# Kernel tuning notes

Hardware: AMD Instinct MI355X
Metric: run time of the kernel (lower is better)

## Reference

```python
import jax, jax.numpy as jnp
from jax import lax
import numpy as np


def _pool_matrix(L, S):
    # AdaptiveAvgPool1d(L -> S): output i averages input [floor(i*L/S), ceil((i+1)*L/S))
    P = np.zeros((S, L), dtype=np.float32)
    for i in range(S):
        s = (i * L) // S
        e = -(-((i + 1) * L) // S)
        P[i, s:e] = 1.0 / (e - s)
    return jnp.asarray(P)


def _gmask_index(Lc, kind):
    idx = jnp.arange(Lc, dtype=jnp.float32)
    ref = float((Lc + 1) // 2 if kind == 'center' else Lc - 1)
    sigma = jnp.mean(jnp.abs(idx - ref))
    w = jnp.exp(-0.5 * (idx - ref) ** 2 / sigma ** 2)
    return w / w.sum()  # (Lc,)


def _gmask_vector(seq, kind):
    Lc = seq.shape[1]
    ref_i = (Lc + 1) // 2 if kind == 'center' else Lc - 1
    diff = seq - seq[:, ref_i, :][:, None, :]
    d = jnp.sqrt(jnp.maximum(jnp.sum(diff * diff, axis=2), 1e-12))  # safe ||.||2
    sigma = jnp.mean(d, axis=1, keepdims=True)
    w = jnp.exp(-0.5 * (d / sigma) ** 2)
    return w / jnp.sum(w, axis=1, keepdims=True)  # (B, Lc)


def _l2norm(w):  # F.normalize(p=2, dim=1)
    return w / jnp.maximum(jnp.linalg.norm(w, axis=1, keepdims=True), 1e-12)


def _dwconv(u, w, b, L):
    # u: (B, len, C); depthwise Conv1d, padding=d_conv-1 both sides, slice [:, :, :L]
    C = u.shape[-1]
    pad = w.shape[-1] - 1
    v = lax.conv_general_dilated(u.transpose(0, 2, 1), w, (1,), [(pad, pad)],
                                 dimension_numbers=('NCH', 'OIH', 'NCH'),
                                 feature_group_count=C)
    v = v + b[None, :, None]
    return v[:, :, :L].transpose(0, 2, 1)


def _ssm(u, W_xp, b_xp, W_dt, b_dt, A_log, D):
    d_state = A_log.shape[1]
    dt_rank = W_dt.shape[1]
    A = -jnp.exp(A_log)                                       # (d_inner, d_state)
    dbc = u @ W_xp.T + b_xp
    dr = dbc[..., :dt_rank]
    Bm = dbc[..., dt_rank:dt_rank + d_state]
    Cm = dbc[..., dt_rank + d_state:]
    delta = jax.nn.softplus(dr @ W_dt.T + b_dt)               # (B, L, d_inner)
    deltaA = jnp.exp(delta[..., None] * A)                    # (B, L, d_inner, d_state)
    BX = (delta * u)[..., None] * Bm[:, :, None, :]           # (B, L, d_inner, d_state)

    def comb(e1, e2):  # h_t = a_t * h_{t-1} + b_t (parallel scan)
        a1, b1 = e1
        a2, b2 = e2
        return a1 * a2, a2 * b1 + b2

    hs = lax.associative_scan(comb, (deltaA, BX), axis=1)[1]
    return jnp.einsum('blds,bls->bld', hs, Cm) + D * u


def _forward(x, W_in_x, W_in_z, conv_w_f, conv_b_f, conv_w_b, conv_b_b,
             W_xp_f, b_xp_f, W_dt_f, b_dt_f, A_log_f, D_f,
             W_xp_b, b_xp_b, W_dt_b, b_dt_b, A_log_b, D_b,
             W_pro_to, b_pro_to, token_wA, token_wV, W_out):
    B, L, Dm = x.shape
    S = token_wA.shape[1]
    xi = x @ W_in_x.T
    z = x @ W_in_z.T
    mid = L // 2 + 1
    x_f = xi[:, :mid]
    x_b = xi[:, mid - 1:][:, ::-1]
    x_f = jax.nn.silu(_dwconv(x_f, conv_w_f, conv_b_f, L))
    x_b = jax.nn.silu(_dwconv(x_b, conv_w_b, conv_b_b, L))
    y_f = _ssm(x_f, W_xp_f, b_xp_f, W_dt_f, b_dt_f, A_log_f, D_f)
    y_b = _ssm(x_b, W_xp_b, b_xp_b, W_dt_b, b_dt_b, A_log_b, D_b)
    Lc = y_f.shape[1]
    m_f = _l2norm(_gmask_index(Lc, 'last')[None, :] * _gmask_vector(y_f, 'last'))
    m_b = _l2norm(_gmask_index(Lc, 'last')[None, :] * _gmask_vector(y_b, 'last'))
    y_cat = jnp.concatenate([y_f * m_f[..., None], y_b * m_b[:, ::-1, None]], axis=-1)
    y = y_cat @ W_pro_to.T + b_pro_to
    m = _l2norm(_gmask_index(Lc, 'center')[None, :] * _gmask_vector(y, 'center'))
    y = y * m[..., None]
    # tokenizer (direction 'f'), dropout is identity at eval
    Atok = jax.nn.softmax(jnp.einsum('bld,td->btl', y, token_wA[0]), axis=-1)
    VV = jnp.einsum('bld,de->ble', y, token_wV[0])
    T = jnp.einsum('btl,ble->bte', Atok, VV)
    # z branch: adaptive avg pool L -> S then silu
    P = _pool_matrix(L, S)
    zp = jax.nn.silu(jnp.einsum('bld,sl->bsd', z, P))
    return (T * zp) @ W_out.T


def setup_inputs() -> dict:
    key = jax.random.key(0)
    B, L, D = 8, 2049, 256
    d_inner, d_state, dt_rank, d_conv, S = 512, 16, 16, 4, 64
    ks = jax.random.split(key, 20)
    rn = lambda k, sh, sc: jax.random.normal(k, sh, jnp.float32) * sc
    A_log = jnp.tile(jnp.log(jnp.arange(1.0, d_state + 1.0, dtype=jnp.float32))[None, :], (d_inner, 1))
    return {
        'x': rn(ks[0], (B, L, D), 1.0),
        'W_in_x': rn(ks[1], (d_inner, D), D ** -0.5),
        'W_in_z': rn(ks[2], (d_inner, D), D ** -0.5),
        'conv_w_f': rn(ks[3], (d_inner, 1, d_conv), 0.5),
        'conv_b_f': rn(ks[4], (d_inner,), 0.1),
        'conv_w_b': rn(ks[5], (d_inner, 1, d_conv), 0.5),
        'conv_b_b': rn(ks[6], (d_inner,), 0.1),
        'W_xp_f': rn(ks[7], (dt_rank + 2 * d_state, d_inner), d_inner ** -0.5),
        'b_xp_f': rn(ks[8], (dt_rank + 2 * d_state,), 0.02),
        'W_dt_f': rn(ks[9], (d_inner, dt_rank), dt_rank ** -0.5),
        'b_dt_f': jax.random.uniform(ks[10], (d_inner,), jnp.float32, -4.0, -2.0),
        'A_log_f': A_log,
        'D_f': jnp.ones((d_inner,), jnp.float32),
        'W_xp_b': rn(ks[11], (dt_rank + 2 * d_state, d_inner), d_inner ** -0.5),
        'b_xp_b': rn(ks[12], (dt_rank + 2 * d_state,), 0.02),
        'W_dt_b': rn(ks[13], (d_inner, dt_rank), dt_rank ** -0.5),
        'b_dt_b': jax.random.uniform(ks[14], (d_inner,), jnp.float32, -4.0, -2.0),
        'A_log_b': A_log,
        'D_b': jnp.ones((d_inner,), jnp.float32),
        'W_pro_to': rn(ks[15], (d_inner, 2 * d_inner), (2 * d_inner) ** -0.5),
        'b_pro_to': jnp.zeros((d_inner,), jnp.float32),
        'token_wA': rn(ks[16], (1, S, d_inner), (2.0 / d_inner) ** 0.5),
        'token_wV': rn(ks[17], (1, d_inner, d_inner), (2.0 / d_inner) ** 0.5),
        'W_out': rn(ks[18], (D, d_inner), d_inner ** -0.5),
    }


def reference(x, W_in_x, W_in_z, conv_w_f, conv_b_f, conv_w_b, conv_b_b,
              W_xp_f, b_xp_f, W_dt_f, b_dt_f, A_log_f, D_f,
              W_xp_b, b_xp_b, W_dt_b, b_dt_b, A_log_b, D_b,
              W_pro_to, b_pro_to, token_wA, token_wV, W_out):
    return _forward(x, W_in_x, W_in_z, conv_w_f, conv_b_f, conv_w_b, conv_b_b,
                    W_xp_f, b_xp_f, W_dt_f, b_dt_f, A_log_f, D_f,
                    W_xp_b, b_xp_b, W_dt_b, b_dt_b, A_log_b, D_b,
                    W_pro_to, b_pro_to, token_wA, token_wV, W_out)
```

## Files before the change

kernel.cpp:

```cpp
#include <hip/hip_runtime.h>
#include <math.h>

#define BB 8
#define LL 2049
#define DD 256
#define EE 512
#define NS 16
#define LC 1028
#define SS 64
#define SC 40
#define CH 26
#define LN2F 0.6931471805599453f

typedef __attribute__((ext_vector_type(8))) short short8x;
typedef __attribute__((ext_vector_type(4))) float f32x4;

__device__ __forceinline__ float4 ld4g(const float* p) { return *(const float4*)p; }

__device__ __forceinline__ unsigned short bfrne(float f)
{
    unsigned int u = __float_as_uint(f);
    unsigned int r = (u + 0x7FFFu + ((u >> 16) & 1u)) >> 16;
    return (unsigned short)r;
}

__device__ __forceinline__ float fast_softplus(float x)
{
    float sp = __log2f(1.f + __expf(x)) * LN2F;
    return x > 8.f ? x + __expf(-x) : sp;
}

__device__ __forceinline__ float fast_silu(float x)
{
    return __fdividef(x, 1.f + __expf(-x));
}

__device__ __forceinline__ void gl_lds16(const unsigned short* g, unsigned short* l)
{
    __builtin_amdgcn_global_load_lds(
        (const __attribute__((address_space(1))) unsigned int*)g,
        (__attribute__((address_space(3))) unsigned int*)l, 16, 0, 0);
}

__device__ __forceinline__ void gemm_bf16_core(
    unsigned short* As, unsigned short* Bs,
    const unsigned short* __restrict__ A, const unsigned short* __restrict__ Bw,
    const float* __restrict__ bias, float* __restrict__ C,
    int M, int N, int K, int ldc)
{
    const int tid = threadIdx.x;
    const int wave = tid >> 6, lane = tid & 63;
    const int quad = lane >> 4, l16 = lane & 15;
    const int m0 = blockIdx.y * 128, n0 = blockIdx.x * 128;
    const int wm = (wave >> 1) * 64, wn = (wave & 1) * 64;
    const int srow = lane >> 2;
    const int skoff = (lane & 3) * 8;

    f32x4 acc[4][4];
#pragma unroll
    for (int i = 0; i < 4; i++)
#pragma unroll
        for (int j = 0; j < 4; j++) { f32x4 z = {0.f, 0.f, 0.f, 0.f}; acc[i][j] = z; }

    for (int k0 = 0; k0 < K; k0 += 32) {
#pragma unroll
        for (int half = 0; half < 2; half++) {
            int r = wave * 32 + half * 16 + srow;
            int ga = m0 + r; if (ga > M - 1) ga = M - 1;
            int gb = n0 + r; if (gb > N - 1) gb = N - 1;
            gl_lds16(A + (size_t)ga * K + k0 + skoff, &As[(wave * 32 + half * 16) * 32]);
            gl_lds16(Bw + (size_t)gb * K + k0 + skoff, &Bs[(wave * 32 + half * 16) * 32]);
        }
        __syncthreads();
        short8x af[4], bf[4];
#pragma unroll
        for (int t = 0; t < 4; t++) {
            af[t] = *(const short8x*)&As[(wm + t * 16 + l16) * 32 + quad * 8];
            bf[t] = *(const short8x*)&Bs[(wn + t * 16 + l16) * 32 + quad * 8];
        }
#pragma unroll
        for (int mt = 0; mt < 4; mt++)
#pragma unroll
            for (int nt = 0; nt < 4; nt++)
                acc[mt][nt] = __builtin_amdgcn_mfma_f32_16x16x32_bf16(
                    af[mt], bf[nt], acc[mt][nt], 0, 0, 0);
        __syncthreads();
    }

#pragma unroll
    for (int mt = 0; mt < 4; mt++) {
#pragma unroll
        for (int r = 0; r < 4; r++) {
            int m = m0 + wm + mt * 16 + quad * 4 + r;
            if (m >= M) continue;
#pragma unroll
            for (int nt = 0; nt < 4; nt++) {
                int n = n0 + wn + nt * 16 + l16;
                if (n >= N) continue;
                float v = acc[mt][nt][r];
                if (bias) v += bias[n];
                C[(size_t)m * ldc + n] = v;
            }
        }
    }
}

__global__ __launch_bounds__(256) void gemm_bf16_bt(
    const unsigned short* __restrict__ A, const unsigned short* __restrict__ Bw,
    const float* __restrict__ bias, float* __restrict__ C,
    int M, int N, int K, int ldc)
{
    __shared__ unsigned short As[128 * 32];
    __shared__ unsigned short Bs[128 * 32];
    gemm_bf16_core(As, Bs, A, Bw, bias, C, M, N, K, ldc);
}

__global__ __launch_bounds__(256) void gemm_bf16_pair(
    const unsigned short* __restrict__ A0, const unsigned short* __restrict__ A1,
    const unsigned short* __restrict__ B0, const unsigned short* __restrict__ B1,
    const float* __restrict__ bias0, const float* __restrict__ bias1,
    float* __restrict__ C0, float* __restrict__ C1,
    int M, int N, int K, int ldc)
{
    __shared__ unsigned short As[128 * 32];
    __shared__ unsigned short Bs[128 * 32];
    int z = blockIdx.z;
    gemm_bf16_core(As, Bs, z ? A1 : A0, z ? B1 : B0, z ? bias1 : bias0,
                   z ? C1 : C0, M, N, K, ldc);
}

__global__ __launch_bounds__(256) void cvt_all(
    const float* __restrict__ s0, unsigned short* __restrict__ d0,
    const float* __restrict__ s1, unsigned short* __restrict__ d1,
    const float* __restrict__ s2, unsigned short* __restrict__ d2,
    const float* __restrict__ s3, unsigned short* __restrict__ d3,
    const float* __restrict__ s4, unsigned short* __restrict__ d4,
    const float* __restrict__ s5, unsigned short* __restrict__ d5,
    const float* __restrict__ s6, unsigned short* __restrict__ d6,
    const float* __restrict__ sV, unsigned short* __restrict__ dV)
{
    __shared__ float tile[32][33];
    if (blockIdx.x < 1024) {
        const size_t c0 = 1049088, c1 = c0 + 32768, c2 = c1 + 32768, c3 = c2 + 6144,
                     c4 = c3 + 6144, c5 = c4 + 131072, c6 = c5 + 8192;
        size_t stride = (size_t)1024 * 256;
        for (size_t i = (size_t)blockIdx.x * 256 + threadIdx.x; i < c6; i += stride) {
            const float* s; unsigned short* d; size_t j;
            if (i < c0)      { s = s0; d = d0; j = i; }
            else if (i < c1) { s = s1; d = d1; j = i - c0; }
            else if (i < c2) { s = s2; d = d2; j = i - c1; }
            else if (i < c3) { s = s3; d = d3; j = i - c2; }
            else if (i < c4) { s = s4; d = d4; j = i - c3; }
            else if (i < c5) { s = s5; d = d5; j = i - c4; }
            else             { s = s6; d = d6; j = i - c5; }
            float4 v = ((const float4*)s)[j];
            ushort4 o;
            o.x = bfrne(v.x); o.y = bfrne(v.y); o.z = bfrne(v.z); o.w = bfrne(v.w);
            ((ushort4*)d)[j] = o;
        }
    } else {
        int t = blockIdx.x - 1024;
        int bx = t & 15, by = t >> 4;
        int tx = threadIdx.x & 31, ty = threadIdx.x >> 5;
        for (int i = 0; i < 32; i += 8)
            tile[ty + i][tx] = sV[(size_t)(by * 32 + ty + i) * 512 + bx * 32 + tx];
        __syncthreads();
        for (int i = 0; i < 32; i += 8)
            dV[(size_t)(bx * 32 + ty + i) * 512 + by * 32 + tx] = bfrne(tile[tx][ty + i]);
    }
}

__global__ __launch_bounds__(256) void gemm_abt(
    const float* __restrict__ A, const float* __restrict__ Bw,
    const float* __restrict__ bias, float* __restrict__ C,
    float* __restrict__ Cpart, int M, int N, int K)
{
    __shared__ float As[16][132];
    __shared__ float Bs[16][132];
    const int tid = threadIdx.x;
    const int tx = tid & 15, ty = tid >> 4;
    const int m0 = blockIdx.y * 128, n0 = blockIdx.x * 128;
    const int Ks = K / gridDim.z;
    const int kbeg = blockIdx.z * Ks, kend = kbeg + Ks;
    const int r0 = tid >> 2, r1 = r0 + 64;
    const int kc = (tid & 3) * 4;

    float acc[8][8];
#pragma unroll
    for (int i = 0; i < 8; i++)
#pragma unroll
        for (int j = 0; j < 8; j++) acc[i][j] = 0.f;

    const float4 z4 = make_float4(0.f, 0.f, 0.f, 0.f);
    float4 a0, a1, b0, b1;
    a0 = (m0 + r0 < M) ? ld4g(A + (size_t)(m0 + r0) * K + kbeg + kc) : z4;
    a1 = (m0 + r1 < M) ? ld4g(A + (size_t)(m0 + r1) * K + kbeg + kc) : z4;
    b0 = (n0 + r0 < N) ? ld4g(Bw + (size_t)(n0 + r0) * K + kbeg + kc) : z4;
    b1 = (n0 + r1 < N) ? ld4g(Bw + (size_t)(n0 + r1) * K + kbeg + kc) : z4;

    for (int k0 = kbeg; k0 < kend; k0 += 16) {
        As[kc + 0][r0] = a0.x; As[kc + 1][r0] = a0.y; As[kc + 2][r0] = a0.z; As[kc + 3][r0] = a0.w;
        As[kc + 0][r1] = a1.x; As[kc + 1][r1] = a1.y; As[kc + 2][r1] = a1.z; As[kc + 3][r1] = a1.w;
        Bs[kc + 0][r0] = b0.x; Bs[kc + 1][r0] = b0.y; Bs[kc + 2][r0] = b0.z; Bs[kc + 3][r0] = b0.w;
        Bs[kc + 0][r1] = b1.x; Bs[kc + 1][r1] = b1.y; Bs[kc + 2][r1] = b1.z; Bs[kc + 3][r1] = b1.w;
        __syncthreads();
        if ((k0 + 16) < kend) {
            int kn = k0 + 16 + kc;
            a0 = (m0 + r0 < M) ? ld4g(A + (size_t)(m0 + r0) * K + kn) : z4;
            a1 = (m0 + r1 < M) ? ld4g(A + (size_t)(m0 + r1) * K + kn) : z4;
            b0 = (n0 + r0 < N) ? ld4g(Bw + (size_t)(n0 + r0) * K + kn) : z4;
            b1 = (n0 + r1 < N) ? ld4g(Bw + (size_t)(n0 + r1) * K + kn) : z4;
        }
#pragma unroll
        for (int kk = 0; kk < 16; kk++) {
            float4 alo = *(const float4*)&As[kk][ty * 4];
            float4 ahi = *(const float4*)&As[kk][64 + ty * 4];
            float4 blo = *(const float4*)&Bs[kk][tx * 4];
            float4 bhi = *(const float4*)&Bs[kk][64 + tx * 4];
            float a[8] = {alo.x, alo.y, alo.z, alo.w, ahi.x, ahi.y, ahi.z, ahi.w};
            float b[8] = {blo.x, blo.y, blo.z, blo.w, bhi.x, bhi.y, bhi.z, bhi.w};
#pragma unroll
            for (int i = 0; i < 8; i++)
#pragma unroll
                for (int j = 0; j < 8; j++) acc[i][j] += a[i] * b[j];
        }
        __syncthreads();
    }

    float* Co = (blockIdx.z == 0) ? C : Cpart + (size_t)(blockIdx.z - 1) * M * N;
    const bool addb = (bias != nullptr) && (blockIdx.z == 0);
#pragma unroll
    for (int i = 0; i < 8; i++) {
        int m = m0 + (i < 4 ? ty * 4 + i : 64 + ty * 4 + i - 4);
        if (m >= M) continue;
#pragma unroll
        for (int jh = 0; jh < 2; jh++) {
            int n = n0 + jh * 64 + tx * 4;
            if (n >= N) continue;
            float4 o;
            o.x = acc[i][jh * 4 + 0]; o.y = acc[i][jh * 4 + 1];
            o.z = acc[i][jh * 4 + 2]; o.w = acc[i][jh * 4 + 3];
            if (addb) {
                o.x += bias[n]; o.y += bias[n + 1];
                o.z += bias[n + 2]; o.w += bias[n + 3];
            }
            *(float4*)(Co + (size_t)m * N + n) = o;
        }
    }
}

__global__ __launch_bounds__(256) void reduce_add(
    float* __restrict__ C, const float* __restrict__ P, int parts, size_t total)
{
    size_t stride = (size_t)gridDim.x * 256 * 4;
    for (size_t i = ((size_t)blockIdx.x * 256 + threadIdx.x) * 4; i < total; i += stride) {
        float4 c = *(float4*)(C + i);
        for (int p = 0; p < parts; p++) {
            float4 v = *(const float4*)(P + (size_t)p * total + i);
            c.x += v.x; c.y += v.y; c.z += v.z; c.w += v.w;
        }
        *(float4*)(C + i) = c;
    }
}

__global__ __launch_bounds__(256) void conv_silu_kernel(
    const float* __restrict__ xi,
    const float* __restrict__ wf, const float* __restrict__ bf,
    const float* __restrict__ wb, const float* __restrict__ bbk,
    float* __restrict__ xfc, float* __restrict__ xbc,
    unsigned short* __restrict__ xfcbf, unsigned short* __restrict__ xbcbf)
{
    int idx = blockIdx.x * 256 + threadIdx.x;
    if (idx >= LC * EE) return;
    int b = blockIdx.y;
    int dir = blockIdx.z;
    int t = idx >> 9;
    int e = idx & 511;
    const float* w = dir ? wb : wf;
    float s = dir ? bbk[e] : bf[e];
#pragma unroll
    for (int k = 0; k < 4; k++) {
        int j = t + k - 3;
        if (j >= 0 && j <= 1024) {
            int src_l = dir ? (2048 - j) : j;
            s += w[e * 4 + k] * xi[((size_t)b * LL + src_l) * EE + e];
        }
    }
    float v = fast_silu(s);
    size_t o = ((size_t)b * LC + t) * EE + e;
    (dir ? xbc : xfc)[o] = v;
    (dir ? xbcbf : xfcbf)[o] = bfrne(v);
}

__device__ __forceinline__ void pow_tree(float r, float* pw)
{
    float r2 = r * r;
    float r4 = r2 * r2;
    float r8 = r4 * r4;
    pw[0] = r;        pw[1] = r2;       pw[2] = r2 * r;   pw[3] = r4;
    pw[4] = r4 * r;   pw[5] = r4 * r2;  pw[6] = r4 * pw[2]; pw[7] = r8;
    pw[8] = r8 * r;   pw[9] = r8 * r2;  pw[10] = r8 * pw[2]; pw[11] = r8 * r4;
    pw[12] = r8 * pw[4]; pw[13] = r8 * pw[5]; pw[14] = r8 * pw[6]; pw[15] = r8 * r8;
}

__global__ __launch_bounds__(256) void scan_phase1(
    const float* __restrict__ xfc, const float* __restrict__ xbc,
    const float* __restrict__ dbcf, const float* __restrict__ dbcb,
    const float* __restrict__ Wdt_f, const float* __restrict__ bdt_f,
    const float* __restrict__ Alog_f,
    const float* __restrict__ Wdt_b, const float* __restrict__ bdt_b,
    const float* __restrict__ Alog_b,
    float* __restrict__ Hloc, float* __restrict__ Dsum)
{
    const int bid = blockIdx.x;
    const int half = bid & 1;
    const int c = (bid >> 1) % SC;
    const int rest = (bid >> 1) / SC;
    const int b = rest & 7;
    const int dir = rest >> 3;
    const int e = half * 256 + threadIdx.x;

    const float* u    = dir ? xbc : xfc;
    const float* dbc  = dir ? dbcb : dbcf;
    const float* Wdt  = dir ? Wdt_b : Wdt_f;
    const float* bdt  = dir ? bdt_b : bdt_f;
    const float* Alog = dir ? Alog_b : Alog_f;

    float W[16], h[16];
#pragma unroll
    for (int i = 0; i < 16; i += 4) {
        float4 w4 = *(const float4*)(Wdt + e * 16 + i);
        W[i] = w4.x; W[i + 1] = w4.y; W[i + 2] = w4.z; W[i + 3] = w4.w;
    }
#pragma unroll
    for (int i = 0; i < 16; i++) h[i] = 0.f;
    float A0 = -__expf(Alog[e * 16]);
    float bd = bdt[e];
    float dsum = 0.f;

    const int l0 = c * CH;
    int l1 = l0 + CH; if (l1 > LC) l1 = LC;
    const float* urow = u + ((size_t)b * LC + l0) * EE + e;
    const float* row  = dbc + ((size_t)b * LC + l0) * 48;

    for (int l = l0; l < l1; ++l, row += 48, urow += EE) {
        float p = bd;
#pragma unroll
        for (int k = 0; k < 16; k++) p += row[k] * W[k];
        float delta = fast_softplus(p);
        dsum += delta;
        float du = delta * (*urow);
        float r = __expf(delta * A0);
        float pw[16];
        pow_tree(r, pw);
#pragma unroll
        for (int n = 0; n < 16; n++) h[n] = pw[n] * h[n] + du * row[16 + n];
    }
    size_t base = ((((size_t)dir * 8 + b) * SC + c) * 16) * 512 + e;
#pragma unroll
    for (int n = 0; n < 16; n++) Hloc[base + (size_t)n * 512] = h[n];
    Dsum[(((size_t)dir * 8 + b) * SC + c) * 512 + e] = dsum;
}

__global__ __launch_bounds__(256) void scan_phase2(
    float* __restrict__ Hloc, const float* __restrict__ Dsum,
    const float* __restrict__ Alog_f, const float* __restrict__ Alog_b)
{
    int gid = blockIdx.x * 256 + threadIdx.x;
    int e = gid & 511;
    int n = (gid >> 9) & 15;
    int b = (gid >> 13) & 7;
    int dir = gid >> 16;
    const float* Alog = dir ? Alog_b : Alog_f;
    float An = -__expf(Alog[e * 16 + n]);
    size_t base = (((size_t)dir * 8 + b) * SC * 16 + n) * 512 + e;
    size_t dbase = ((size_t)dir * 8 + b) * SC * 512 + e;
    float h = 0.f;
#pragma unroll
    for (int c = 0; c < SC; c++) {
        size_t off = base + (size_t)c * 16 * 512;
        float tmp = Hloc[off];
        float P = __expf(Dsum[dbase + (size_t)c * 512] * An);
        Hloc[off] = h;
        h = P * h + tmp;
    }
}

__global__ __launch_bounds__(256) void scan_phase3(
    const float* __restrict__ xfc, const float* __restrict__ xbc,
    const float* __restrict__ dbcf, const float* __restrict__ dbcb,
    const float* __restrict__ Wdt_f, const float* __restrict__ bdt_f,
    const float* __restrict__ Alog_f, const float* __restrict__ Df,
    const float* __restrict__ Wdt_b, const float* __restrict__ bdt_b,
    const float* __restrict__ Alog_b, const float* __restrict__ Db,
    const float* __restrict__ Hin,
    float* __restrict__ yf, float* __restrict__ yb)
{
    const int bid = blockIdx.x;
    const int half = bid & 1;
    const int c = (bid >> 1) % SC;
    const int rest = (bid >> 1) / SC;
    const int b = rest & 7;
    const int dir = rest >> 3;
    const int e = half * 256 + threadIdx.x;

    const float* u    = dir ? xbc : xfc;
    const float* dbc  = dir ? dbcb : dbcf;
    const float* Wdt  = dir ? Wdt_b : Wdt_f;
    const float* bdt  = dir ? bdt_b : bdt_f;
    const float* Alog = dir ? Alog_b : Alog_f;
    const float* Dp   = dir ? Db : Df;
    float* y          = dir ? yb : yf;

    float W[16], h[16];
#pragma unroll
    for (int i = 0; i < 16; i += 4) {
        float4 w4 = *(const float4*)(Wdt + e * 16 + i);
        W[i] = w4.x; W[i + 1] = w4.y; W[i + 2] = w4.z; W[i + 3] = w4.w;
    }
    float A0 = -__expf(Alog[e * 16]);
    float bd = bdt[e];
    float Dv = Dp[e];
    size_t hbase = ((((size_t)dir * 8 + b) * SC + c) * 16) * 512 + e;
#pragma unroll
    for (int n = 0; n < 16; n++) h[n] = Hin[hbase + (size_t)n * 512];

    const int l0 = c * CH;
    int l1 = l0 + CH; if (l1 > LC) l1 = LC;
    const float* urow = u + ((size_t)b * LC + l0) * EE + e;
    float* yrow       = y + ((size_t)b * LC + l0) * EE + e;
    const float* row  = dbc + ((size_t)b * LC + l0) * 48;

    for (int l = l0; l < l1; ++l, row += 48, urow += EE, yrow += EE) {
        float p = bd;
#pragma unroll
        for (int k = 0; k < 16; k++) p += row[k] * W[k];
        float delta = fast_softplus(p);
        float uv = *urow;
        float du = delta * uv;
        float r = __expf(delta * A0);
        float pw[16];
        pow_tree(r, pw);
        float q0 = 0.f, q1 = 0.f, q2 = 0.f, q3 = 0.f;
#pragma unroll
        for (int i = 0; i < 4; i++) {
#pragma unroll
            for (int j = 0; j < 4; j++) {
                int n = i * 4 + j;
                h[n] = pw[n] * h[n] + du * row[16 + n];
            }
            q0 += h[i * 4 + 0] * row[32 + i * 4 + 0];
            q1 += h[i * 4 + 1] * row[32 + i * 4 + 1];
            q2 += h[i * 4 + 2] * row[32 + i * 4 + 2];
            q3 += h[i * 4 + 3] * row[32 + i * 4 + 3];
        }
        *yrow = ((q0 + q1) + (q2 + q3)) + Dv * uv;
    }
}

__global__ __launch_bounds__(256) void dist2_kernel(
    const float* __restrict__ Y0, const float* __restrict__ Y1,
    float* __restrict__ D0, float* __restrict__ D1, int ref_l)
{
    const float* Y = blockIdx.z ? Y1 : Y0;
    float* dbuf = blockIdx.z ? D1 : D0;
    int wave = threadIdx.x >> 6;
    int lane = threadIdx.x & 63;
    int l = blockIdx.x * 4 + wave;
    int b = blockIdx.y;
    if (l >= LC) return;
    const float* row = Y + ((size_t)b * LC + l) * EE;
    const float* ref = Y + ((size_t)b * LC + ref_l) * EE;
    float s = 0.f;
#pragma unroll
    for (int i = 0; i < 8; i += 4) {
        float4 a = *(const float4*)(row + lane * 8 + i);
        float4 r = *(const float4*)(ref + lane * 8 + i);
        float dx = a.x - r.x, dy = a.y - r.y, dz = a.z - r.z, dw = a.w - r.w;
        s += dx * dx + dy * dy + dz * dz + dw * dw;
    }
    for (int m = 1; m < 64; m <<= 1) s += __shfl_xor(s, m, 64);
    if (lane == 0) dbuf[(size_t)b * LC + l] = sqrtf(fmaxf(s, 1e-12f));
}

__device__ __forceinline__ float block_reduce_sum256(float v, float* red)
{
    int tid = threadIdx.x;
    red[tid] = v; __syncthreads();
    for (int s = 128; s > 0; s >>= 1) {
        if (tid < s) red[tid] += red[tid + s];
        __syncthreads();
    }
    float r = red[0]; __syncthreads();
    return r;
}

__global__ __launch_bounds__(256) void mask_finalize2(
    const float* __restrict__ db0, const float* __restrict__ db1,
    float* __restrict__ mb0, float* __restrict__ mb1, float ref)
{
    __shared__ float red[256];
    int b = blockIdx.x, tid = threadIdx.x;
    const float* d = (blockIdx.y ? db1 : db0) + (size_t)b * LC;
    float* m = (blockIdx.y ? mb1 : mb0) + (size_t)b * LC;
    float s1 = 0.f, s2 = 0.f;
    for (int l = tid; l < LC; l += 256) {
        s1 += d[l];
        s2 += fabsf((float)l - ref);
    }
    float sigma = block_reduce_sum256(s1, red) / (float)LC;
    float si    = block_reduce_sum256(s2, red) / (float)LC;
    float invsg = 1.f / sigma, invsi = 1.f / si;
    float s3 = 0.f, s4 = 0.f;
    for (int l = tid; l < LC; l += 256) {
        float t1 = d[l] * invsg;             s3 += __expf(-0.5f * t1 * t1);
        float t2 = ((float)l - ref) * invsi; s4 += __expf(-0.5f * t2 * t2);
    }
    float invwv = 1.f / block_reduce_sum256(s3, red);
    float invwi = 1.f / block_reduce_sum256(s4, red);
    float s5 = 0.f;
    for (int l = tid; l < LC; l += 256) {
        float t1 = d[l] * invsg;             float gv = __expf(-0.5f * t1 * t1) * invwv;
        float t2 = ((float)l - ref) * invsi; float gi = __expf(-0.5f * t2 * t2) * invwi;
        float v = gi * gv; s5 += v * v;
    }
    float invn = 1.f / fmaxf(sqrtf(block_reduce_sum256(s5, red)), 1e-12f);
    for (int l = tid; l < LC; l += 256) {
        float t1 = d[l] * invsg;             float gv = __expf(-0.5f * t1 * t1) * invwv;
        float t2 = ((float)l - ref) * invsi; float gi = __expf(-0.5f * t2 * t2) * invwi;
        m[l] = (gi * gv) * invn;
    }
}

__global__ __launch_bounds__(256) void build_ycat_bf16(
    const float* __restrict__ yf, const float* __restrict__ yb,
    const float* __restrict__ mf, const float* __restrict__ mb,
    unsigned short* __restrict__ ycat)
{
    size_t idx = (size_t)blockIdx.x * 256 + threadIdx.x;
    if (idx >= (size_t)BB * LC * EE) return;
    int e = (int)(idx & 511);
    size_t bl = idx >> 9;
    int l = (int)(bl % LC);
    int b = (int)(bl / LC);
    size_t rl = (size_t)b * LC + (LC - 1 - l);
    ycat[bl * 1024 + e] = bfrne(yf[idx] * mf[bl]);
    ycat[bl * 1024 + 512 + e] = bfrne(yb[idx] * mb[rl]);
}

__global__ __launch_bounds__(256) void apply_mask_bf16(
    const float* __restrict__ y, const float* __restrict__ mc,
    unsigned short* __restrict__ ybf)
{
    size_t idx = (size_t)blockIdx.x * 256 + threadIdx.x;
    if (idx >= (size_t)BB * LC * EE) return;
    ybf[idx] = bfrne(y[idx] * mc[idx >> 9]);
}

__global__ __launch_bounds__(256) void softmax_l(float* __restrict__ logits)
{
    __shared__ float red[256];
    int b = blockIdx.x >> 6, t = blockIdx.x & 63;
    int tid = threadIdx.x;
    float* base = logits + (size_t)b * LC * 576 + t;
    float mx = -1e30f;
    for (int l = tid; l < LC; l += 256) mx = fmaxf(mx, base[(size_t)l * 576]);
    red[tid] = mx; __syncthreads();
    for (int s = 128; s > 0; s >>= 1) {
        if (tid < s) red[tid] = fmaxf(red[tid], red[tid + s]);
        __syncthreads();
    }
    mx = red[0]; __syncthreads();
    float sum = 0.f;
    for (int l = tid; l < LC; l += 256) sum += __expf(base[(size_t)l * 576] - mx);
    red[tid] = sum; __syncthreads();
    for (int s = 128; s > 0; s >>= 1) {
        if (tid < s) red[tid] += red[tid + s];
        __syncthreads();
    }
    float inv = 1.f / red[0];
    for (int l = tid; l < LC; l += 256)
        base[(size_t)l * 576] = __expf(base[(size_t)l * 576] - mx) * inv;
}

__global__ __launch_bounds__(256) void t_kernel(
    const float* __restrict__ cc, const float* __restrict__ zp,
    float* __restrict__ T)
{
    __shared__ float As[16][64];
    int b = blockIdx.y;
    int e0 = blockIdx.x * 64;
    int lbeg = blockIdx.z * 129;
    int lend = lbeg + 129; if (lend > LC) lend = LC;
    int tid = threadIdx.x;
    int el = tid & 63;
    int tq = tid >> 6;
    float acc[16];
#pragma unroll
    for (int j = 0; j < 16; j++) acc[j] = 0.f;
    for (int l0 = lbeg; l0 < lend; l0 += 16) {
        int lld = tid >> 4;
        int tld = (tid & 15) * 4;
        int l = l0 + lld;
        float4 v = make_float4(0.f, 0.f, 0.f, 0.f);
        if (l < lend) v = *(const float4*)(cc + ((size_t)b * LC + l) * 576 + tld);
        *(float4*)&As[lld][tld] = v;
        __syncthreads();
        int lmax = lend - l0 < 16 ? lend - l0 : 16;
        for (int i = 0; i < lmax; i++) {
            float vvv = cc[((size_t)b * LC + l0 + i) * 576 + 64 + e0 + el];
#pragma unroll
            for (int j = 0; j < 16; j++) acc[j] += As[i][tq * 16 + j] * vvv;
        }
        __syncthreads();
    }
#pragma unroll
    for (int j = 0; j < 16; j++) {
        size_t o = ((size_t)b * 64 + tq * 16 + j) * EE + e0 + el;
        atomicAdd(&T[o], acc[j] * zp[o]);
    }
}

__global__ __launch_bounds__(256) void zp_kernel(
    const float* __restrict__ z, float* __restrict__ zp, float* __restrict__ T)
{
    int s = blockIdx.x, b = blockIdx.y;
    int tid = threadIdx.x;
    {
        size_t base = ((size_t)b * SS + s) * 512;
        *(float4*)(T + base + tid * 2) = make_float4(0.f, 0.f, 0.f, 0.f);
    }
    int si = (s * LL) / SS;
    int ei = ((s + 1) * LL + SS - 1) / SS;
    float inv = 1.f / (float)(ei - si);
    for (int d = tid; d < EE; d += 256) {
        float acc = 0.f;
        for (int l = si; l < ei; l++) acc += z[((size_t)b * LL + l) * EE + d];
        zp[((size_t)b * SS + s) * EE + d] = fast_silu(acc * inv);
    }
}

extern "C" void kernel_launch(void* const* d_in, const int* in_sizes, int n_in,
                              void* d_out, int out_size, void* d_ws, size_t ws_size,
                              hipStream_t stream)
{
    const float* x        = (const float*)d_in[0];
    const float* W_in_x   = (const float*)d_in[1];
    const float* W_in_z   = (const float*)d_in[2];
    const float* conv_w_f = (const float*)d_in[3];
    const float* conv_b_f = (const float*)d_in[4];
    const float* conv_w_b = (const float*)d_in[5];
    const float* conv_b_b = (const float*)d_in[6];
    const float* W_xp_f   = (const float*)d_in[7];
    const float* b_xp_f   = (const float*)d_in[8];
    const float* W_dt_f   = (const float*)d_in[9];
    const float* b_dt_f   = (const float*)d_in[10];
    const float* A_log_f  = (const float*)d_in[11];
    const float* D_f      = (const float*)d_in[12];
    const float* W_xp_b   = (const float*)d_in[13];
    const float* b_xp_b   = (const float*)d_in[14];
    const float* W_dt_b   = (const float*)d_in[15];
    const float* b_dt_b   = (const float*)d_in[16];
    const float* A_log_b  = (const float*)d_in[17];
    const float* D_b      = (const float*)d_in[18];
    const float* W_pro    = (const float*)d_in[19];
    const float* b_pro    = (const float*)d_in[20];
    const float* token_wA = (const float*)d_in[21];
    const float* token_wV = (const float*)d_in[22];
    const float* W_out    = (const float*)d_in[23];
    float* out = (float*)d_out;
    float* ws  = (float*)d_ws;

    const size_t n1 = (size_t)BB * LL * EE;
    const size_t n2 = (size_t)BB * LC * EE;
    const size_t n3 = (size_t)BB * LC * 48;
    const size_t n4 = (size_t)BB * LC;
    const size_t n6 = (size_t)BB * SS * EE;
    const size_t nHl = (size_t)2 * BB * SC * 16 * 512;

    float* z_buf  = ws;
    float* xi     = z_buf + n1;
    float* xfc    = xi + n1;
    float* xbc    = xfc + n2;
    float* dbcf   = xbc + n2;
    float* dbcb   = dbcf + n3;
    float* yb_buf = dbcb + n3;
    float* y_buf  = yb_buf + n2;
    float* mf     = y_buf + n2;
    float* mb     = mf + n4;
    float* mc     = mb + n4;
    float* d1     = mc + n4;
    float* d2     = d1 + n4;
    float* T_buf  = d2 + n4;
    float* zp_buf = T_buf + n6;
    float* wA_reg = zp_buf + n6;
    float* wvt_reg = wA_reg + 16384;
    size_t need = (size_t)(wvt_reg + 131072 - ws) * sizeof(float);
    if (ws_size < need) return;

    float* Hloc   = xi;
    float* Dsum   = xi + nHl;
    float* Cc     = xi;
    float* yf_buf = y_buf;
    unsigned short* xbf    = (unsigned short*)y_buf;
    unsigned short* xfcbf  = (unsigned short*)y_buf;
    unsigned short* xbcbf  = xfcbf + n2;
    unsigned short* wbf1   = (unsigned short*)yb_buf;
    unsigned short* wbf2   = (unsigned short*)(yb_buf + 65536);
    unsigned short* wxpfbf = (unsigned short*)(yb_buf + 131072);
    unsigned short* wxpbbf = (unsigned short*)(yb_buf + 143360);
    unsigned short* wprobf = (unsigned short*)zp_buf;
    unsigned short* ycatbf = (unsigned short*)xfc;
    unsigned short* ybf    = (unsigned short*)xbc;
    unsigned short* wABbf  = (unsigned short*)wA_reg;
    unsigned short* wAbf   = wABbf;
    unsigned short* wvtbf  = wABbf + 32768;

    dim3 blk(256);

    cvt_all<<<dim3(1280), blk, 0, stream>>>(
        x, xbf, W_in_x, wbf1, W_in_z, wbf2, W_xp_f, wxpfbf, W_xp_b, wxpbbf,
        W_pro, wprobf, token_wA, wAbf, token_wV, wvtbf);
    gemm_bf16_pair<<<dim3(4, 129, 2), blk, 0, stream>>>(
        xbf, xbf, wbf1, wbf2, nullptr, nullptr, xi, z_buf, BB * LL, EE, DD, EE);
    conv_silu_kernel<<<dim3((LC * EE) / 256, BB, 2), blk, 0, stream>>>(
        xi, conv_w_f, conv_b_f, conv_w_b, conv_b_b, xfc, xbc, xfcbf, xbcbf);
    gemm_bf16_pair<<<dim3(1, 65, 2), blk, 0, stream>>>(
        xfcbf, xbcbf, wxpfbf, wxpbbf, b_xp_f, b_xp_b, dbcf, dbcb,
        BB * LC, 48, EE, 48);
    scan_phase1<<<dim3(1280), blk, 0, stream>>>(xfc, xbc, dbcf, dbcb,
        W_dt_f, b_dt_f, A_log_f, W_dt_b, b_dt_b, A_log_b, Hloc, Dsum);
    scan_phase2<<<dim3(512), blk, 0, stream>>>(Hloc, Dsum, A_log_f, A_log_b);
    scan_phase3<<<dim3(1280), blk, 0, stream>>>(xfc, xbc, dbcf, dbcb,
        W_dt_f, b_dt_f, A_log_f, D_f, W_dt_b, b_dt_b, A_log_b, D_b, Hloc,
        yf_buf, yb_buf);
    dist2_kernel<<<dim3(257, BB, 2), blk, 0, stream>>>(yf_buf, yb_buf, d1, d2, LC - 1);
    mask_finalize2<<<dim3(BB, 2), blk, 0, stream>>>(d1, d2, mf, mb, (float)(LC - 1));
    build_ycat_bf16<<<dim3(16448), blk, 0, stream>>>(yf_buf, yb_buf, mf, mb, ycatbf);
    gemm_bf16_bt<<<dim3(4, 65), blk, 0, stream>>>(ycatbf, wprobf, b_pro, y_buf,
                                                  BB * LC, EE, 2 * EE, EE);
    dist2_kernel<<<dim3(257, BB, 1), blk, 0, stream>>>(y_buf, y_buf, d1, d1, (LC + 1) / 2);
    mask_finalize2<<<dim3(BB, 1), blk, 0, stream>>>(d1, d1, mc, mc, (float)((LC + 1) / 2));
    apply_mask_bf16<<<dim3(16448), blk, 0, stream>>>(y_buf, mc, ybf);
    gemm_bf16_bt<<<dim3(5, 65), blk, 0, stream>>>(ybf, wABbf, nullptr, Cc,
                                                  BB * LC, 576, EE, 576);
    softmax_l<<<dim3(BB * SS), blk, 0, stream>>>(Cc);
    zp_kernel<<<dim3(SS, BB), blk, 0, stream>>>(z_buf, zp_buf, T_buf);
    t_kernel<<<dim3(8, BB, 8), blk, 0, stream>>>(Cc, zp_buf, T_buf);
    gemm_abt<<<dim3(2, 4, 4), blk, 0, stream>>>(T_buf, W_out, nullptr, out, yb_buf, BB * SS, DD, EE);
    reduce_add<<<dim3(128), blk, 0, stream>>>(out, yb_buf, 3, (size_t)BB * SS * DD);
}
```

Before: 455.4 us.

## Store input-projection outputs and conv activations in bf16 to cut memory traffic

The paired input-projection GEMM now writes xi and z directly as bf16. The conv+SiLU kernel reads bf16, processes four channels per thread with vector loads, and writes only the bf16 result. The scan kernels and the pooling kernel read these bf16 activations instead of fp32 copies, and workspace buffers are reassigned to match. This halves the bytes moved for several large intermediates and drops the duplicate fp32 output of the conv, at the cost of extra rounding error in z, xi and the scan inputs.

```diff
diff --git a/kernel.cpp b/kernel.cpp
--- a/kernel.cpp
+++ b/kernel.cpp
@@ -24,6 +24,11 @@
     return (unsigned short)r;
 }
 
+__device__ __forceinline__ float bf2f(unsigned short u)
+{
+    return __uint_as_float((unsigned int)u << 16);
+}
+
 __device__ __forceinline__ float fast_softplus(float x)
 {
     float sp = __log2f(1.f + __expf(x)) * LN2F;
@@ -42,10 +47,11 @@
         (__attribute__((address_space(3))) unsigned int*)l, 16, 0, 0);
 }
 
+template<bool OBF>
 __device__ __forceinline__ void gemm_bf16_core(
     unsigned short* As, unsigned short* Bs,
     const unsigned short* __restrict__ A, const unsigned short* __restrict__ Bw,
-    const float* __restrict__ bias, float* __restrict__ C,
+    const float* __restrict__ bias, void* __restrict__ C,
     int M, int N, int K, int ldc)
 {
     const int tid = threadIdx.x;
@@ -99,7 +105,8 @@
                 if (n >= N) continue;
                 float v = acc[mt][nt][r];
                 if (bias) v += bias[n];
-                C[(size_t)m * ldc + n] = v;
+                if (OBF) ((unsigned short*)C)[(size_t)m * ldc + n] = bfrne(v);
+                else     ((float*)C)[(size_t)m * ldc + n] = v;
             }
         }
     }
@@ -112,7 +119,7 @@
 {
     __shared__ unsigned short As[128 * 32];
     __shared__ unsigned short Bs[128 * 32];
-    gemm_bf16_core(As, Bs, A, Bw, bias, C, M, N, K, ldc);
+    gemm_bf16_core<false>(As, Bs, A, Bw, bias, C, M, N, K, ldc);
 }
 
 __global__ __launch_bounds__(256) void gemm_bf16_pair(
@@ -125,8 +132,21 @@
     __shared__ unsigned short As[128 * 32];
     __shared__ unsigned short Bs[128 * 32];
     int z = blockIdx.z;
-    gemm_bf16_core(As, Bs, z ? A1 : A0, z ? B1 : B0, z ? bias1 : bias0,
-                   z ? C1 : C0, M, N, K, ldc);
+    gemm_bf16_core<false>(As, Bs, z ? A1 : A0, z ? B1 : B0, z ? bias1 : bias0,
+                          z ? C1 : C0, M, N, K, ldc);
+}
+
+__global__ __launch_bounds__(256) void gemm_bf16_pair_obf(
+    const unsigned short* __restrict__ A0, const unsigned short* __restrict__ A1,
+    const unsigned short* __restrict__ B0, const unsigned short* __restrict__ B1,
+    unsigned short* __restrict__ C0, unsigned short* __restrict__ C1,
+    int M, int N, int K, int ldc)
+{
+    __shared__ unsigned short As[128 * 32];
+    __shared__ unsigned short Bs[128 * 32];
+    int z = blockIdx.z;
+    gemm_bf16_core<true>(As, Bs, z ? A1 : A0, z ? B1 : B0, nullptr,
+                         z ? C1 : C0, M, N, K, ldc);
 }
 
 __global__ __launch_bounds__(256) void cvt_all(
@@ -264,32 +284,44 @@
 }
 
 __global__ __launch_bounds__(256) void conv_silu_kernel(
-    const float* __restrict__ xi,
+    const unsigned short* __restrict__ xi,
     const float* __restrict__ wf, const float* __restrict__ bf,
     const float* __restrict__ wb, const float* __restrict__ bbk,
-    float* __restrict__ xfc, float* __restrict__ xbc,
     unsigned short* __restrict__ xfcbf, unsigned short* __restrict__ xbcbf)
 {
     int idx = blockIdx.x * 256 + threadIdx.x;
-    if (idx >= LC * EE) return;
+    if (idx >= LC * (EE / 4)) return;
     int b = blockIdx.y;
     int dir = blockIdx.z;
-    int t = idx >> 9;
-    int e = idx & 511;
+    int t = idx >> 7;
+    int e0 = (idx & 127) * 4;
     const float* w = dir ? wb : wf;
-    float s = dir ? bbk[e] : bf[e];
+    float4 w0 = *(const float4*)(w + (e0 + 0) * 4);
+    float4 w1 = *(const float4*)(w + (e0 + 1) * 4);
+    float4 w2 = *(const float4*)(w + (e0 + 2) * 4);
+    float4 w3 = *(const float4*)(w + (e0 + 3) * 4);
+    float4 bias = *(const float4*)((dir ? bbk : bf) + e0);
+    float s0 = bias.x, s1 = bias.y, s2 = bias.z, s3 = bias.w;
 #pragma unroll
     for (int k = 0; k < 4; k++) {
         int j = t + k - 3;
         if (j >= 0 && j <= 1024) {
             int src_l = dir ? (2048 - j) : j;
-            s += w[e * 4 + k] * xi[((size_t)b * LL + src_l) * EE + e];
-        }
-    }
-    float v = fast_silu(s);
-    size_t o = ((size_t)b * LC + t) * EE + e;
-    (dir ? xbc : xfc)[o] = v;
-    (dir ? xbcbf : xfcbf)[o] = bfrne(v);
+            ushort4 u4 = *(const ushort4*)(xi + ((size_t)b * LL + src_l) * EE + e0);
+            float wk0 = (k == 0) ? w0.x : (k == 1) ? w0.y : (k == 2) ? w0.z : w0.w;
+            float wk1 = (k == 0) ? w1.x : (k == 1) ? w1.y : (k == 2) ? w1.z : w1.w;
+            float wk2 = (k == 0) ? w2.x : (k == 1) ? w2.y : (k == 2) ? w2.z : w2.w;
+            float wk3 = (k == 0) ? w3.x : (k == 1) ? w3.y : (k == 2) ? w3.z : w3.w;
+            s0 += wk0 * bf2f(u4.x);
+            s1 += wk1 * bf2f(u4.y);
+            s2 += wk2 * bf2f(u4.z);
+            s3 += wk3 * bf2f(u4.w);
+        }
+    }
+    ushort4 o;
+    o.x = bfrne(fast_silu(s0)); o.y = bfrne(fast_silu(s1));
+    o.z = bfrne(fast_silu(s2)); o.w = bfrne(fast_silu(s3));
+    *(ushort4*)((dir ? xbcbf : xfcbf) + ((size_t)b * LC + t) * EE + e0) = o;
 }
 
 __device__ __forceinline__ void pow_tree(float r, float* pw)
@@ -304,7 +336,7 @@
 }
 
 __global__ __launch_bounds__(256) void scan_phase1(
-    const float* __restrict__ xfc, const float* __restrict__ xbc,
+    const unsigned short* __restrict__ xfc, const unsigned short* __restrict__ xbc,
     const float* __restrict__ dbcf, const float* __restrict__ dbcb,
     const float* __restrict__ Wdt_f, const float* __restrict__ bdt_f,
     const float* __restrict__ Alog_f,
@@ -320,7 +352,7 @@
     const int dir = rest >> 3;
     const int e = half * 256 + threadIdx.x;
 
-    const float* u    = dir ? xbc : xfc;
+    const unsigned short* u = dir ? xbc : xfc;
     const float* dbc  = dir ? dbcb : dbcf;
     const float* Wdt  = dir ? Wdt_b : Wdt_f;
     const float* bdt  = dir ? bdt_b : bdt_f;
@@ -340,7 +372,7 @@
 
     const int l0 = c * CH;
     int l1 = l0 + CH; if (l1 > LC) l1 = LC;
-    const float* urow = u + ((size_t)b * LC + l0) * EE + e;
+    const unsigned short* urow = u + ((size_t)b * LC + l0) * EE + e;
     const float* row  = dbc + ((size_t)b * LC + l0) * 48;
 
     for (int l = l0; l < l1; ++l, row += 48, urow += EE) {
@@ -349,7 +381,7 @@
         for (int k = 0; k < 16; k++) p += row[k] * W[k];
         float delta = fast_softplus(p);
         dsum += delta;
-        float du = delta * (*urow);
+        float du = delta * bf2f(*urow);
         float r = __expf(delta * A0);
         float pw[16];
         pow_tree(r, pw);
@@ -387,7 +419,7 @@
 }
 
 __global__ __launch_bounds__(256) void scan_phase3(
-    const float* __restrict__ xfc, const float* __restrict__ xbc,
+    const unsigned short* __restrict__ xfc, const unsigned short* __restrict__ xbc,
     const float* __restrict__ dbcf, const float* __restrict__ dbcb,
     const float* __restrict__ Wdt_f, const float* __restrict__ bdt_f,
     const float* __restrict__ Alog_f, const float* __restrict__ Df,
@@ -404,7 +436,7 @@
     const int dir = rest >> 3;
     const int e = half * 256 + threadIdx.x;
 
-    const float* u    = dir ? xbc : xfc;
+    const unsigned short* u = dir ? xbc : xfc;
     const float* dbc  = dir ? dbcb : dbcf;
     const float* Wdt  = dir ? Wdt_b : Wdt_f;
     const float* bdt  = dir ? bdt_b : bdt_f;
@@ -427,7 +459,7 @@
 
     const int l0 = c * CH;
     int l1 = l0 + CH; if (l1 > LC) l1 = LC;
-    const float* urow = u + ((size_t)b * LC + l0) * EE + e;
+    const unsigned short* urow = u + ((size_t)b * LC + l0) * EE + e;
     float* yrow       = y + ((size_t)b * LC + l0) * EE + e;
     const float* row  = dbc + ((size_t)b * LC + l0) * 48;
 
@@ -436,7 +468,7 @@
 #pragma unroll
         for (int k = 0; k < 16; k++) p += row[k] * W[k];
         float delta = fast_softplus(p);
-        float uv = *urow;
+        float uv = bf2f(*urow);
         float du = delta * uv;
         float r = __expf(delta * A0);
         float pw[16];
@@ -622,7 +654,8 @@
 }
 
 __global__ __launch_bounds__(256) void zp_kernel(
-    const float* __restrict__ z, float* __restrict__ zp, float* __restrict__ T)
+    const unsigned short* __restrict__ z, float* __restrict__ zp,
+    float* __restrict__ T)
 {
     int s = blockIdx.x, b = blockIdx.y;
     int tid = threadIdx.x;
@@ -635,7 +668,7 @@
     float inv = 1.f / (float)(ei - si);
     for (int d = tid; d < EE; d += 256) {
         float acc = 0.f;
-        for (int l = si; l < ei; l++) acc += z[((size_t)b * LL + l) * EE + d];
+        for (int l = si; l < ei; l++) acc += bf2f(z[((size_t)b * LL + l) * EE + d]);
         zp[((size_t)b * SS + s) * EE + d] = fast_silu(acc * inv);
     }
 }
@@ -684,8 +717,8 @@
     float* xbc    = xfc + n2;
     float* dbcf   = xbc + n2;
     float* dbcb   = dbcf + n3;
-    float* yb_buf = dbcb + n3;
-    float* y_buf  = yb_buf + n2;
+    float* yb_reg = dbcb + n3;
+    float* y_buf  = yb_reg + n2;
     float* mf     = y_buf + n2;
     float* mb     = mf + n4;
     float* mc     = mb + n4;
@@ -698,19 +731,22 @@
     size_t need = (size_t)(wvt_reg + 131072 - ws) * sizeof(float);
     if (ws_size < need) return;
 
+    unsigned short* xi_bf  = (unsigned short*)xi;
+    unsigned short* z_bf   = (unsigned short*)z_buf;
     float* Hloc   = xi;
     float* Dsum   = xi + nHl;
     float* Cc     = xi;
-    float* yf_buf = y_buf;
+    float* yf_buf = xfc;
+    float* yb_buf = xbc;
     unsigned short* xbf    = (unsigned short*)y_buf;
     unsigned short* xfcbf  = (unsigned short*)y_buf;
     unsigned short* xbcbf  = xfcbf + n2;
-    unsigned short* wbf1   = (unsigned short*)yb_buf;
-    unsigned short* wbf2   = (unsigned short*)(yb_buf + 65536);
-    unsigned short* wxpfbf = (unsigned short*)(yb_buf + 131072);
-    unsigned short* wxpbbf = (unsigned short*)(yb_buf + 143360);
+    unsigned short* wbf1   = (unsigned short*)yb_reg;
+    unsigned short* wbf2   = (unsigned short*)(yb_reg + 65536);
+    unsigned short* wxpfbf = (unsigned short*)(yb_reg + 131072);
+    unsigned short* wxpbbf = (unsigned short*)(yb_reg + 143360);
     unsigned short* wprobf = (unsigned short*)zp_buf;
-    unsigned short* ycatbf = (unsigned short*)xfc;
+    unsigned short* ycatbf = (unsigned short*)yb_reg;
     unsigned short* ybf    = (unsigned short*)xbc;
     unsigned short* wABbf  = (unsigned short*)wA_reg;
     unsigned short* wAbf   = wABbf;
@@ -721,17 +757,17 @@
     cvt_all<<<dim3(1280), blk, 0, stream>>>(
         x, xbf, W_in_x, wbf1, W_in_z, wbf2, W_xp_f, wxpfbf, W_xp_b, wxpbbf,
         W_pro, wprobf, token_wA, wAbf, token_wV, wvtbf);
-    gemm_bf16_pair<<<dim3(4, 129, 2), blk, 0, stream>>>(
-        xbf, xbf, wbf1, wbf2, nullptr, nullptr, xi, z_buf, BB * LL, EE, DD, EE);
-    conv_silu_kernel<<<dim3((LC * EE) / 256, BB, 2), blk, 0, stream>>>(
-        xi, conv_w_f, conv_b_f, conv_w_b, conv_b_b, xfc, xbc, xfcbf, xbcbf);
+    gemm_bf16_pair_obf<<<dim3(4, 129, 2), blk, 0, stream>>>(
+        xbf, xbf, wbf1, wbf2, xi_bf, z_bf, BB * LL, EE, DD, EE);
+    conv_silu_kernel<<<dim3(514, BB, 2), blk, 0, stream>>>(
+        xi_bf, conv_w_f, conv_b_f, conv_w_b, conv_b_b, xfcbf, xbcbf);
     gemm_bf16_pair<<<dim3(1, 65, 2), blk, 0, stream>>>(
         xfcbf, xbcbf, wxpfbf, wxpbbf, b_xp_f, b_xp_b, dbcf, dbcb,
         BB * LC, 48, EE, 48);
-    scan_phase1<<<dim3(1280), blk, 0, stream>>>(xfc, xbc, dbcf, dbcb,
+    scan_phase1<<<dim3(1280), blk, 0, stream>>>(xfcbf, xbcbf, dbcf, dbcb,
         W_dt_f, b_dt_f, A_log_f, W_dt_b, b_dt_b, A_log_b, Hloc, Dsum);
     scan_phase2<<<dim3(512), blk, 0, stream>>>(Hloc, Dsum, A_log_f, A_log_b);
-    scan_phase3<<<dim3(1280), blk, 0, stream>>>(xfc, xbc, dbcf, dbcb,
+    scan_phase3<<<dim3(1280), blk, 0, stream>>>(xfcbf, xbcbf, dbcf, dbcb,
         W_dt_f, b_dt_f, A_log_f, D_f, W_dt_b, b_dt_b, A_log_b, D_b, Hloc,
         yf_buf, yb_buf);
     dist2_kernel<<<dim3(257, BB, 2), blk, 0, stream>>>(yf_buf, yb_buf, d1, d2, LC - 1);
@@ -745,8 +781,8 @@
     gemm_bf16_bt<<<dim3(5, 65), blk, 0, stream>>>(ybf, wABbf, nullptr, Cc,
                                                   BB * LC, 576, EE, 576);
     softmax_l<<<dim3(BB * SS), blk, 0, stream>>>(Cc);
-    zp_kernel<<<dim3(SS, BB), blk, 0, stream>>>(z_buf, zp_buf, T_buf);
+    zp_kernel<<<dim3(SS, BB), blk, 0, stream>>>(z_bf, zp_buf, T_buf);
     t_kernel<<<dim3(8, BB, 8), blk, 0, stream>>>(Cc, zp_buf, T_buf);
-    gemm_abt<<<dim3(2, 4, 4), blk, 0, stream>>>(T_buf, W_out, nullptr, out, yb_buf, BB * SS, DD, EE);
-    reduce_add<<<dim3(128), blk, 0, stream>>>(out, yb_buf, 3, (size_t)BB * SS * DD);
-}
+    gemm_abt<<<dim3(2, 4, 4), blk, 0, stream>>>(T_buf, W_out, nullptr, out, yb_reg, BB * SS, DD, EE);
+    reduce_add<<<dim3(128), blk, 0, stream>>>(out, yb_reg, 3, (size_t)BB * SS * DD);
+}
```

Result: faster. 438.1 us (-3.8%).
